# Kernel tuning notes

Hardware: AMD Instinct MI355X
Metric: run time of the kernel (lower is better)

## Reference

```python
import jax, jax.numpy as jnp
import numpy as np

B, U, V = 2, 32, 2048
IN_DIM, STATE, CODE = 256, 512, 256
H, HD = 8, 64
INNER = H * HD  # 512
HID = STATE     # ffn capacity_factor = 1.0


def layernorm(x, g, b, eps=1e-5):
    mu = jnp.mean(x, axis=-1, keepdims=True)
    var = jnp.var(x, axis=-1, keepdims=True)
    return (x - mu) * jax.lax.rsqrt(var + eps) * g + b


def setup_inputs() -> dict:
    key = jax.random.key(0)
    ks = jax.random.split(key, 24)
    s = 0.02
    inp = {
        'receiver_states': jax.random.normal(ks[0], (B, U, STATE), jnp.float32),
        'receiver_signatures': jax.random.normal(ks[1], (B, U, 64), jnp.float32),
        'receiver_codes': jax.random.normal(ks[2], (B, U, CODE), jnp.float32),
        'sender_states': jax.random.normal(ks[3], (B, V, IN_DIM), jnp.float32),
        # layernorms
        'ln_s_g': jnp.ones((IN_DIM,), jnp.float32), 'ln_s_b': jnp.zeros((IN_DIM,), jnp.float32),
        'ln_r_g': jnp.ones((STATE,), jnp.float32), 'ln_r_b': jnp.zeros((STATE,), jnp.float32),
        # ModFC query: in=STATE out=INNER ctx=CODE
        'Wq': jax.random.normal(ks[4], (INNER, STATE), jnp.float32) * s,
        'bq': jnp.zeros((INNER,), jnp.float32),
        'Cq': jax.random.normal(ks[5], (STATE, CODE), jnp.float32) * s,
        # ModFC key/value: in=IN_DIM out=INNER ctx=CODE
        'Wk': jax.random.normal(ks[6], (INNER, IN_DIM), jnp.float32) * s,
        'bk': jnp.zeros((INNER,), jnp.float32),
        'Ck': jax.random.normal(ks[7], (IN_DIM, CODE), jnp.float32) * s,
        'Wv': jax.random.normal(ks[8], (INNER, IN_DIM), jnp.float32) * s,
        'bv': jnp.zeros((INNER,), jnp.float32),
        'Cv': jax.random.normal(ks[9], (IN_DIM, CODE), jnp.float32) * s,
        # exit ModFC: in=INNER out=STATE ctx=CODE
        'We': jax.random.normal(ks[10], (STATE, INNER), jnp.float32) * s,
        'be': jnp.zeros((STATE,), jnp.float32),
        'Ce': jax.random.normal(ks[11], (INNER, CODE), jnp.float32) * s,
        'ls_attn': jnp.ones((STATE,), jnp.float32) * 1.0,
        # FFN
        'ln_f_g': jnp.ones((STATE,), jnp.float32), 'ln_f_b': jnp.zeros((STATE,), jnp.float32),
        'W1': jax.random.normal(ks[12], (HID, STATE), jnp.float32) * s,
        'b1': jnp.zeros((HID,), jnp.float32),
        'C1': jax.random.normal(ks[13], (STATE, CODE), jnp.float32) * s,
        'W2': jax.random.normal(ks[14], (STATE, HID), jnp.float32) * s,
        'b2': jnp.zeros((STATE,), jnp.float32),
        'C2': jax.random.normal(ks[15], (HID, CODE), jnp.float32) * s,
        'ls_ffn': jnp.ones((STATE,), jnp.float32) * 1e-6,
    }
    return inp


def reference(receiver_states, receiver_signatures, receiver_codes, sender_states,
              ln_s_g, ln_s_b, ln_r_g, ln_r_b,
              Wq, bq, Cq, Wk, bk, Ck, Wv, bv, Cv, We, be, Ce, ls_attn,
              ln_f_g, ln_f_b, W1, b1, C1, W2, b2, C2, ls_ffn):
    codes = receiver_codes  # (b,u,code)
    # --- ReadInAttention ---
    r_ln = layernorm(receiver_states, ln_r_g, ln_r_b)           # (b,u,state)
    s_ln = layernorm(sender_states, ln_s_g, ln_s_b)             # (b,v,in)
    # ModFC: y = linear(x * (1 + code @ C))
    # queries: (b,u,inner)
    q = jnp.einsum('bus,is->bui', r_ln * (1.0 + jnp.einsum('buc,sc->bus', codes, Cq)), Wq) + bq
    # per-receiver modulated senders: scale (b,u,in) broadcast over v
    scale_k = 1.0 + jnp.einsum('buc,ic->bui', codes, Ck)        # (b,u,in)
    scale_v = 1.0 + jnp.einsum('buc,ic->bui', codes, Cv)        # (b,u,in)
    mod_k = s_ln[:, :, None, :] * scale_k[:, None, :, :]        # (b,v,u,in)
    mod_v = s_ln[:, :, None, :] * scale_v[:, None, :, :]        # (b,v,u,in)
    keys = jnp.einsum('bvui,oi->bvuo', mod_k, Wk) + bk          # (b,v,u,inner)
    values = jnp.einsum('bvui,oi->bvuo', mod_v, Wv) + bv        # (b,v,u,inner)
    keys = keys.reshape(B, V, U, H, HD).transpose(0, 3, 2, 1, 4)    # (b,h,u,v,c)
    values = values.reshape(B, V, U, H, HD).transpose(0, 3, 2, 1, 4)
    qh = q.reshape(B, U, H, HD).transpose(0, 2, 1, 3)           # (b,h,u,c)
    scores = jnp.einsum('bhuc,bhuvc->bhuv', qh, keys) / np.sqrt(HD)
    attn = jax.nn.softmax(scores, axis=-1)
    msg = jnp.einsum('bhuv,bhuvc->bhuc', attn, values)          # (b,h,u,c)
    msg = msg.transpose(0, 2, 1, 3).reshape(B, U, INNER)        # (b,u,inner)
    msg = jnp.einsum('bui,oi->buo', msg * (1.0 + jnp.einsum('buc,ic->bui', codes, Ce)), We) + be
    attn_out = msg * ls_attn  # include_residual=False in read-in attention
    # --- ModFFN (residual) ---
    x = attn_out
    r = layernorm(x, ln_f_g, ln_f_b)
    h1 = jnp.einsum('bus,os->buo', r * (1.0 + jnp.einsum('buc,sc->bus', codes, C1)), W1) + b1
    h1 = jax.nn.gelu(h1, approximate=False)
    h2 = jnp.einsum('buh,oh->buo', h1 * (1.0 + jnp.einsum('buc,hc->buh', codes, C2)), W2) + b2
    out = x + h2 * ls_ffn
    return out
```

## Files before the change

kernel.cpp:

```cpp
#include <hip/hip_runtime.h>
#include <math.h>

#define B_ 2
#define U_ 32
#define V_ 2048
#define IN_ 256
#define ST_ 512
#define H_ 8
#define BU_ 64
#define NR_ 512

#define WS_SLN   0u
#define WS_SLNT  1048576u
#define WS_SCALE 2097152u
#define WS_T     2260992u
#define WS_CB    2392064u
#define WS_SSUMP 2392576u
#define WS_CTXP  2396672u
#define WS_AO    3445248u
#define WS_H2    3478016u
#define WS_AOP   3510784u

__device__ __forceinline__ float wsum(float v){
  #pragma unroll
  for(int m=32;m>0;m>>=1) v += __shfl_xor(v, m, 64);
  return v;
}

#define FMA4(A, t, S) { A.x += (t)*(S).x; A.y += (t)*(S).y; A.z += (t)*(S).z; A.w += (t)*(S).w; }

__global__ __launch_bounds__(256) void k_pre(const float* __restrict__ snd,
    const float* __restrict__ g, const float* __restrict__ bb,
    const float* __restrict__ codes,
    const float* __restrict__ Cq, const float* __restrict__ Ck, const float* __restrict__ Cv,
    const float* __restrict__ Ce, const float* __restrict__ C1, const float* __restrict__ C2,
    float* __restrict__ ws){
  __shared__ float tile[32][261];
  __shared__ float cds[8][256];
  const int tid = threadIdx.x;
  if(blockIdx.x < 128){
    const int wave = tid>>6, lane = tid&63;
    const int rowbase = blockIdx.x * 32;
    const int b = rowbase >> 11, vloc = rowbase & 2047;
    float4 gg  = *(const float4*)(g  + lane*4);
    float4 bbv = *(const float4*)(bb + lane*4);
    for(int it=0; it<8; ++it){
      int rl = it*4 + wave;
      int r  = rowbase + rl;
      float4 x = *(const float4*)(snd + (size_t)r*IN_ + lane*4);
      float s = x.x+x.y+x.z+x.w;
      float q = x.x*x.x+x.y*x.y+x.z*x.z+x.w*x.w;
      s = wsum(s); q = wsum(q);
      float mu = s*(1.0f/256.0f);
      float rv = rsqrtf(q*(1.0f/256.0f) - mu*mu + 1e-5f);
      float4 y;
      y.x = (x.x-mu)*rv*gg.x + bbv.x;
      y.y = (x.y-mu)*rv*gg.y + bbv.y;
      y.z = (x.z-mu)*rv*gg.z + bbv.z;
      y.w = (x.w-mu)*rv*gg.w + bbv.w;
      *(float4*)(ws + WS_SLN + (size_t)r*IN_ + lane*4) = y;
      tile[rl][lane*4+0] = y.x;
      tile[rl][lane*4+1] = y.y;
      tile[rl][lane*4+2] = y.z;
      tile[rl][lane*4+3] = y.w;
    }
    __syncthreads();
    const int vh = tid & 31;
    const int ibase = (tid >> 5);
    for(int it=0; it<32; ++it){
      int i = it*8 + ibase;
      ws[WS_SLNT + ((size_t)b*IN_ + i)*V_ + vloc + vh] = tile[vh][i];
    }
  } else {
    const int idx = blockIdx.x - 128;
    const int cg = idx % 40, bg = idx / 40;
    #pragma unroll
    for(int j=0;j<8;++j){
      int fi = j*256 + tid;
      cds[fi>>8][fi&255] = codes[(size_t)(bg*8)*256 + fi];
    }
    __syncthreads();
    const int q = tid & 3;
    const int col = cg*64 + (tid >> 2);
    const float* Cp; int loc;
    if(col < 512){ Cp = Cq; loc = col; }
    else if(col < 768){ Cp = Ck; loc = col - 512; }
    else if(col < 1024){ Cp = Cv; loc = col - 768; }
    else if(col < 1536){ Cp = Ce; loc = col - 1024; }
    else if(col < 2048){ Cp = C1; loc = col - 1536; }
    else { Cp = C2; loc = col - 2048; }
    const float4* wrow = (const float4*)(Cp + (size_t)loc*256 + q*64);
    float acc[8] = {0,0,0,0,0,0,0,0};
    #pragma unroll 4
    for(int i=0;i<16;++i){
      float4 w = wrow[i];
      #pragma unroll
      for(int k=0;k<8;++k){
        const float4 c = *(const float4*)(&cds[k][q*64 + i*4]);
        acc[k] += w.x*c.x + w.y*c.y + w.z*c.z + w.w*c.w;
      }
    }
    #pragma unroll
    for(int k=0;k<8;++k){
      acc[k] += __shfl_xor(acc[k], 1, 64);
      acc[k] += __shfl_xor(acc[k], 2, 64);
    }
    ws[WS_SCALE + (size_t)(bg*8 + q)*2560 + col]     = 1.0f + acc[q];
    ws[WS_SCALE + (size_t)(bg*8 + q + 4)*2560 + col] = 1.0f + acc[q+4];
  }
}

__global__ __launch_bounds__(256) void k_qt(const float* __restrict__ rst,
    const float* __restrict__ lg, const float* __restrict__ lb,
    const float* __restrict__ Wq, const float* __restrict__ bq,
    const float* __restrict__ Wk, const float* __restrict__ bk,
    float* __restrict__ ws){
  const int bu = blockIdx.x >> 3, h = blockIdx.x & 7;
  const int b = bu >> 5, u = bu & 31;
  const int r = (b*8 + h)*32 + u;
  const int tid = threadIdx.x, wave = tid>>6, lane = tid&63;
  __shared__ float xm[512];
  __shared__ float qv[64];
  __shared__ float red[4][65];
  __shared__ float rsm[4], rqm[4];
  float2 x2 = *(const float2*)(rst + (size_t)bu*512 + tid*2);
  float s = x2.x + x2.y, q = x2.x*x2.x + x2.y*x2.y;
  s = wsum(s); q = wsum(q);
  if(lane==0){ rsm[wave] = s; rqm[wave] = q; }
  __syncthreads();
  float S = rsm[0]+rsm[1]+rsm[2]+rsm[3];
  float Q = rqm[0]+rqm[1]+rqm[2]+rqm[3];
  float mu = S*(1.0f/512.0f);
  float rv = rsqrtf(Q*(1.0f/512.0f) - mu*mu + 1e-5f);
  const float* scal = ws + WS_SCALE + (size_t)bu*2560;
  xm[tid*2]   = ((x2.x-mu)*rv*lg[tid*2]   + lb[tid*2])   * scal[tid*2];
  xm[tid*2+1] = ((x2.y-mu)*rv*lg[tid*2+1] + lb[tid*2+1]) * scal[tid*2+1];
  __syncthreads();
  {
    const int o = tid & 63, sp = tid >> 6;
    const float4* wq = (const float4*)(Wq + (size_t)(h*64 + o)*512 + sp*128);
    const float* xp = xm + sp*128;
    float acc = 0.f;
    #pragma unroll 8
    for(int c4=0;c4<32;++c4){
      float4 w = wq[c4];
      acc += w.x*xp[c4*4] + w.y*xp[c4*4+1] + w.z*xp[c4*4+2] + w.w*xp[c4*4+3];
    }
    red[sp][o] = acc;
  }
  __syncthreads();
  if(tid < 64)
    qv[tid] = red[0][tid]+red[1][tid]+red[2][tid]+red[3][tid] + bq[h*64+tid];
  __syncthreads();
  if(tid < 64){
    float p = qv[tid] * bk[h*64+tid];
    p = wsum(p);
    if(tid==0) ws[WS_CB + r] = p;
  }
  {
    float acc = 0.f;
    #pragma unroll 4
    for(int d=0; d<64; ++d)
      acc += qv[d] * Wk[(size_t)(h*64+d)*256 + tid];
    ws[WS_T + (size_t)r*256 + tid] = acc * scal[512 + tid];
  }
}

__global__ __launch_bounds__(512) void k_scctx(const float* __restrict__ Tm, float* __restrict__ ws){
  const int rg = blockIdx.x >> 3, vc = blockIdx.x & 7;
  const int r0 = rg * 8;
  const int b  = rg >> 5;
  const int v0 = vc * 256;
  const int tid = threadIdx.x, lane = tid & 63;
  const int w  = __builtin_amdgcn_readfirstlane(tid >> 6);
  const int wr = w & 1, wk = w >> 1;
  const int rw4 = wr * 4;
  const int i0 = lane * 4;
  const int srow = tid >> 6;
  const int sf   = (tid & 63) * 4;

  __shared__ float P[8][256];
  __shared__ float stg[32][256];

  float4 a0={0,0,0,0},a1={0,0,0,0},a2={0,0,0,0},a3={0,0,0,0};
  const float* Trow = Tm + (size_t)(r0 + rw4)*256;

  const float* p1base = ws + WS_SLNT + (size_t)b*IN_*V_ + v0;
  float4 g0,g1,g2,g3;
  g0 = *(const float4*)(p1base + (size_t)(srow    )*V_ + sf);
  g1 = *(const float4*)(p1base + (size_t)(srow+ 8)*V_ + sf);
  g2 = *(const float4*)(p1base + (size_t)(srow+16)*V_ + sf);
  g3 = *(const float4*)(p1base + (size_t)(srow+24)*V_ + sf);
  for(int s=0; s<8; ++s){
    __syncthreads();
    *(float4*)&stg[srow   ][sf] = g0;
    *(float4*)&stg[srow+ 8][sf] = g1;
    *(float4*)&stg[srow+16][sf] = g2;
    *(float4*)&stg[srow+24][sf] = g3;
    if(s < 7){
      const float* nb = p1base + (size_t)(s+1)*32*V_;
      g0 = *(const float4*)(nb + (size_t)(srow    )*V_ + sf);
      g1 = *(const float4*)(nb + (size_t)(srow+ 8)*V_ + sf);
      g2 = *(const float4*)(nb + (size_t)(srow+16)*V_ + sf);
      g3 = *(const float4*)(nb + (size_t)(srow+24)*V_ + sf);
    }
    const int kgA = s*32 + wk*8;
    float4 tA[4], tB[4];
    #pragma unroll
    for(int j=0;j<4;++j) tA[j] = *(const float4*)(Trow + (size_t)j*256 + kgA);
    __syncthreads();
    #pragma unroll
    for(int j=0;j<4;++j) tB[j] = *(const float4*)(Trow + (size_t)j*256 + kgA + 4);
    {
      const int kl = wk*8;
      float4 s0 = *(const float4*)&stg[kl+0][i0];
// ... 86 lines not shown
      FMA4(a3,p3_.x,s0) FMA4(a3,p3_.y,s1) FMA4(a3,p3_.z,s2) FMA4(a3,p3_.w,s3)
    }
  }
  __syncthreads();
  if(wk == 0){
    *(float4*)&P[rw4+0][i0]=a0; *(float4*)&P[rw4+1][i0]=a1;
    *(float4*)&P[rw4+2][i0]=a2; *(float4*)&P[rw4+3][i0]=a3;
  } else if(wk == 1){
    *(float4*)&stg[rw4+0][i0]=a0; *(float4*)&stg[rw4+1][i0]=a1;
    *(float4*)&stg[rw4+2][i0]=a2; *(float4*)&stg[rw4+3][i0]=a3;
  } else if(wk == 2){
    *(float4*)&stg[8+rw4+0][i0]=a0; *(float4*)&stg[8+rw4+1][i0]=a1;
    *(float4*)&stg[8+rw4+2][i0]=a2; *(float4*)&stg[8+rw4+3][i0]=a3;
  }
  __syncthreads();
  if(wk == 3){
    float4 av[4] = {a0,a1,a2,a3};
    #pragma unroll
    for(int j=0;j<4;++j){
      const int r = r0 + rw4 + j;
      float4 q0 = *(const float4*)&P[rw4+j][i0];
      float4 q1 = *(const float4*)&stg[rw4+j][i0];
      float4 q2 = *(const float4*)&stg[8+rw4+j][i0];
      float4 d;
      d.x = av[j].x+q0.x+q1.x+q2.x;
      d.y = av[j].y+q0.y+q1.y+q2.y;
      d.z = av[j].z+q0.z+q1.z+q2.z;
      d.w = av[j].w+q0.w+q1.w+q2.w;
      *(float4*)(ws + WS_CTXP + ((size_t)vc*NR_ + r)*IN_ + i0) = d;
    }
  }
}

__global__ __launch_bounds__(512) void k_mexit(const float* __restrict__ Wv, const float* __restrict__ bv,
    const float* __restrict__ We, float* __restrict__ ws){
  const int bu = blockIdx.x >> 2, st = blockIdx.x & 3;
  const int b = bu >> 5, u = bu & 31;
  const int tid = threadIdx.x;
  __shared__ float xs[2][256];
  __shared__ float m2s[128];
  __shared__ float ps[4][128];
  __shared__ float invS[2];
  if(tid < 2){
    const int r = (b*8 + st*2 + tid)*32 + u;
    float v = 0.f;
    #pragma unroll
    for(int k=0;k<8;++k) v += ws[WS_SSUMP + (size_t)r*8 + k];
    invS[tid] = 1.0f / v;
  }
  {
    const int hh = tid >> 8, i = tid & 255;
    const int r = (b*8 + st*2 + hh)*32 + u;
    float s = 0.f;
    #pragma unroll
    for(int vcx=0; vcx<8; ++vcx)
      s += ws[WS_CTXP + ((size_t)vcx*NR_ + r)*IN_ + i];
    xs[hh][i] = s * ws[WS_SCALE + (size_t)bu*2560 + 768 + i];
  }
  __syncthreads();
  {
    const int lo = tid & 127, sp = tid >> 7;
    const int o = st*128 + lo;
    const float4* wv = (const float4*)(Wv + (size_t)o*256 + sp*64);
    const float* xp = &xs[lo>>6][sp*64];
    float acc = 0.f;
    #pragma unroll
    for(int c4=0;c4<16;++c4){
      float4 w = wv[c4];
      acc += w.x*xp[c4*4]+w.y*xp[c4*4+1]+w.z*xp[c4*4+2]+w.w*xp[c4*4+3];
    }
    ps[sp][lo] = acc;
  }
  __syncthreads();
  if(tid < 128){
    const int o = st*128 + tid;
    m2s[tid] = ((ps[0][tid]+ps[1][tid]+ps[2][tid]+ps[3][tid]) * invS[tid>>6] + bv[o])
               * ws[WS_SCALE + (size_t)bu*2560 + 1024 + o];
  }
  __syncthreads();
  {
    const float4* we = (const float4*)(We + (size_t)tid*512 + st*128);
    float acc = 0.f;
    #pragma unroll 8
    for(int c4=0;c4<32;++c4){
      float4 w = we[c4];
      acc += w.x*m2s[c4*4]+w.y*m2s[c4*4+1]+w.z*m2s[c4*4+2]+w.w*m2s[c4*4+3];
    }
    ws[WS_AOP + ((size_t)st*BU_ + bu)*512 + tid] = acc;
  }
}

__global__ __launch_bounds__(256) void k_ffn1(const float* __restrict__ be, const float* __restrict__ lsa,
    const float* __restrict__ lg, const float* __restrict__ lb,
    const float* __restrict__ W1, const float* __restrict__ b1, float* __restrict__ ws){
  const int bu = blockIdx.x >> 2, ot = blockIdx.x & 3;
  const int tid = threadIdx.x, wave = tid>>6, lane = tid&63;
  __shared__ float xr[512];
  __shared__ float rsm[4], rqm[4];
  __shared__ float ps[2][128];
  const int s2 = tid*2;
  float2 x2;
  {
    const float* aop = ws + WS_AOP;
    float ax = aop[((size_t)0*BU_+bu)*512+s2] + aop[((size_t)1*BU_+bu)*512+s2]
             + aop[((size_t)2*BU_+bu)*512+s2] + aop[((size_t)3*BU_+bu)*512+s2];
    float ay = aop[((size_t)0*BU_+bu)*512+s2+1] + aop[((size_t)1*BU_+bu)*512+s2+1]
             + aop[((size_t)2*BU_+bu)*512+s2+1] + aop[((size_t)3*BU_+bu)*512+s2+1];
    x2.x = (ax + be[s2])   * lsa[s2];
    x2.y = (ay + be[s2+1]) * lsa[s2+1];
    *(float2*)(ws + WS_AO + (size_t)bu*512 + s2) = x2;
  }
  float s = x2.x+x2.y, q = x2.x*x2.x+x2.y*x2.y;
  s = wsum(s); q = wsum(q);
  if(lane==0){ rsm[wave]=s; rqm[wave]=q; }
  __syncthreads();
  float S=rsm[0]+rsm[1]+rsm[2]+rsm[3], Q=rqm[0]+rqm[1]+rqm[2]+rqm[3];
  float mu = S*(1.0f/512.0f);
  float rv = rsqrtf(Q*(1.0f/512.0f) - mu*mu + 1e-5f);
  const float* scal = ws + WS_SCALE + (size_t)bu*2560;
  xr[s2]   = ((x2.x-mu)*rv*lg[s2]   + lb[s2])   * scal[1536 + s2];
  xr[s2+1] = ((x2.y-mu)*rv*lg[s2+1] + lb[s2+1]) * scal[1536 + s2+1];
  __syncthreads();
  const int o = ot*128 + (tid & 127), sp = tid >> 7;
  const float4* w1 = (const float4*)(W1 + (size_t)o*512 + sp*256);
  const float* xp = xr + sp*256;
  float acc = 0.f;
  #pragma unroll 8
  for(int c4=0;c4<64;++c4){
    float4 w = w1[c4];
    acc += w.x*xp[c4*4]+w.y*xp[c4*4+1]+w.z*xp[c4*4+2]+w.w*xp[c4*4+3];
  }
  ps[sp][tid&127] = acc;
  __syncthreads();
  if(sp==0){
    float hh = ps[0][tid] + ps[1][tid] + b1[o];
    float ge = 0.5f*hh*(1.0f + erff(hh*0.70710678118654752f));
    ws[WS_H2 + (size_t)bu*512 + o] = ge * scal[2048 + o];
  }
}

__global__ __launch_bounds__(256) void k_ffn2(const float* __restrict__ W2, const float* __restrict__ b2,
    const float* __restrict__ lsf, const float* __restrict__ ws, float* __restrict__ out){
  const int bu = blockIdx.x >> 2, st = blockIdx.x & 3;
  const int tid = threadIdx.x;
  const int s = st*128 + (tid & 127), sp = tid >> 7;
  __shared__ float ps[2][128];
  const float4* w2 = (const float4*)(W2 + (size_t)s*512 + sp*256);
  const float* hp = ws + WS_H2 + (size_t)bu*512 + sp*256;
  float acc = 0.f;
  #pragma unroll 8
  for(int c4=0;c4<64;++c4){
    float4 w = w2[c4];
    acc += w.x*hp[c4*4]+w.y*hp[c4*4+1]+w.z*hp[c4*4+2]+w.w*hp[c4*4+3];
  }
  ps[sp][tid&127] = acc;
  __syncthreads();
  if(sp==0)
    out[(size_t)bu*512 + s] = ws[WS_AO + (size_t)bu*512 + s]
                            + (ps[0][tid]+ps[1][tid] + b2[s]) * lsf[s];
}

extern "C" void kernel_launch(void* const* d_in, const int* in_sizes, int n_in,
                              void* d_out, int out_size, void* d_ws, size_t ws_size,
                              hipStream_t stream) {
  (void)in_sizes; (void)n_in; (void)out_size; (void)ws_size;
  const float* rst   = (const float*)d_in[0];
  const float* codes = (const float*)d_in[2];
  const float* snd   = (const float*)d_in[3];
  const float* ln_s_g = (const float*)d_in[4];
  const float* ln_s_b = (const float*)d_in[5];
  const float* ln_r_g = (const float*)d_in[6];
  const float* ln_r_b = (const float*)d_in[7];
  const float* Wq = (const float*)d_in[8];
  const float* bq = (const float*)d_in[9];
  const float* Cq = (const float*)d_in[10];
  const float* Wk = (const float*)d_in[11];
  const float* bk = (const float*)d_in[12];
  const float* Ck = (const float*)d_in[13];
  const float* Wv = (const float*)d_in[14];
  const float* bv = (const float*)d_in[15];
  const float* Cv = (const float*)d_in[16];
  const float* We = (const float*)d_in[17];
  const float* be = (const float*)d_in[18];
  const float* Ce = (const float*)d_in[19];
  const float* lsa = (const float*)d_in[20];
  const float* ln_f_g = (const float*)d_in[21];
  const float* ln_f_b = (const float*)d_in[22];
  const float* W1 = (const float*)d_in[23];
  const float* b1 = (const float*)d_in[24];
  const float* C1 = (const float*)d_in[25];
  const float* W2 = (const float*)d_in[26];
  const float* b2 = (const float*)d_in[27];
  const float* C2 = (const float*)d_in[28];
  const float* lsf = (const float*)d_in[29];
  float* ws  = (float*)d_ws;
  float* out = (float*)d_out;

  k_pre   <<<448, 256, 0, stream>>>(snd, ln_s_g, ln_s_b, codes, Cq, Ck, Cv, Ce, C1, C2, ws);
  k_qt    <<<512, 256, 0, stream>>>(rst, ln_r_g, ln_r_b, Wq, bq, Wk, bk, ws);
  k_scctx <<<512, 512, 0, stream>>>((const float*)(ws + WS_T), ws);
  k_mexit <<<256, 512, 0, stream>>>(Wv, bv, We, ws);
  k_ffn1  <<<256, 256, 0, stream>>>(be, lsa, ln_f_g, ln_f_b, W1, b1, ws);
  k_ffn2  <<<256, 256, 0, stream>>>(W2, b2, lsf, ws, out);
}
```

Before: 94.18 us.

## Fuse query/T prep into preprocessing kernel and collapse tail into one per-row kernel

Merges the code-scale computation, receiver layernorm, query projection and key-fold (T) into the sender-layernorm kernel, and fuses value projection, exit projection and both FFN layers into a single per-(b,u) kernel. This cuts the launch count from six to three and removes global round trips through the workspace for scales, attention-out partials and FFN hidden state. The cost is far fewer blocks in the tail (64) and in the query path (64 blocks of 512 threads), each doing full 512x512 matvecs serially. That lowers parallelism and spreads weight reads across only 64 CUs.

After: 240.2 us. +155.0%, slower.

```diff
diff --git a/kernel.cpp b/kernel.cpp
--- a/kernel.cpp
+++ b/kernel.cpp
@@ -12,14 +12,10 @@
 
 #define WS_SLN   0u
 #define WS_SLNT  1048576u
-#define WS_SCALE 2097152u
 #define WS_T     2260992u
 #define WS_CB    2392064u
 #define WS_SSUMP 2392576u
 #define WS_CTXP  2396672u
-#define WS_AO    3445248u
-#define WS_H2    3478016u
-#define WS_AOP   3510784u
 
 __device__ __forceinline__ float wsum(float v){
   #pragma unroll
@@ -29,23 +25,30 @@
 
 #define FMA4(A, t, S) { A.x += (t)*(S).x; A.y += (t)*(S).y; A.z += (t)*(S).z; A.w += (t)*(S).w; }
 
-__global__ __launch_bounds__(256) void k_pre(const float* __restrict__ snd,
-    const float* __restrict__ g, const float* __restrict__ bb,
+__global__ __launch_bounds__(512) void k_pre2(
+    const float* __restrict__ snd, const float* __restrict__ sg, const float* __restrict__ sb,
+    const float* __restrict__ rst, const float* __restrict__ rg, const float* __restrict__ rb,
     const float* __restrict__ codes,
-    const float* __restrict__ Cq, const float* __restrict__ Ck, const float* __restrict__ Cv,
-    const float* __restrict__ Ce, const float* __restrict__ C1, const float* __restrict__ C2,
+    const float* __restrict__ Cq, const float* __restrict__ Ck,
+    const float* __restrict__ Wq, const float* __restrict__ bq,
+    const float* __restrict__ Wk, const float* __restrict__ bk,
     float* __restrict__ ws){
   __shared__ float tile[32][261];
-  __shared__ float cds[8][256];
-  const int tid = threadIdx.x;
+  __shared__ float cds[256];
+  __shared__ float scq[512];
+  __shared__ float sck[256];
+  __shared__ float xm[512];
+  __shared__ float qv[512];
+  __shared__ float rsm[8], rqm[8];
+  const int tid = threadIdx.x, lane = tid & 63, wave = tid >> 6;
   if(blockIdx.x < 128){
-    const int wave = tid>>6, lane = tid&63;
     const int rowbase = blockIdx.x * 32;
     const int b = rowbase >> 11, vloc = rowbase & 2047;
-    float4 gg  = *(const float4*)(g  + lane*4);
-    float4 bbv = *(const float4*)(bb + lane*4);
-    for(int it=0; it<8; ++it){
-      int rl = it*4 + wave;
+    float4 gg  = *(const float4*)(sg + lane*4);
+    float4 bbv = *(const float4*)(sb + lane*4);
+    #pragma unroll
+    for(int it=0; it<4; ++it){
+      int rl = it*8 + wave;
       int r  = rowbase + rl;
       float4 x = *(const float4*)(snd + (size_t)r*IN_ + lane*4);
       float s = x.x+x.y+x.z+x.w;
@@ -65,104 +68,85 @@
       tile[rl][lane*4+3] = y.w;
     }
     __syncthreads();
-    const int vh = tid & 31;
-    const int ibase = (tid >> 5);
-    for(int it=0; it<32; ++it){
-      int i = it*8 + ibase;
+    const int vh = tid & 31, ig = tid >> 5;
+    #pragma unroll
+    for(int it=0; it<16; ++it){
+      int i = it*16 + ig;
       ws[WS_SLNT + ((size_t)b*IN_ + i)*V_ + vloc + vh] = tile[vh][i];
     }
   } else {
-    const int idx = blockIdx.x - 128;
-    const int cg = idx % 40, bg = idx / 40;
-    #pragma unroll
-    for(int j=0;j<8;++j){
-      int fi = j*256 + tid;
-      cds[fi>>8][fi&255] = codes[(size_t)(bg*8)*256 + fi];
-    }
-    __syncthreads();
-    const int q = tid & 3;
-    const int col = cg*64 + (tid >> 2);
-    const float* Cp; int loc;
-    if(col < 512){ Cp = Cq; loc = col; }
-    else if(col < 768){ Cp = Ck; loc = col - 512; }
-    else if(col < 1024){ Cp = Cv; loc = col - 768; }
-    else if(col < 1536){ Cp = Ce; loc = col - 1024; }
-    else if(col < 2048){ Cp = C1; loc = col - 1536; }
-    else { Cp = C2; loc = col - 2048; }
-    const float4* wrow = (const float4*)(Cp + (size_t)loc*256 + q*64);
-    float acc[8] = {0,0,0,0,0,0,0,0};
-    #pragma unroll 4
-    for(int i=0;i<16;++i){
-      float4 w = wrow[i];
+    const int bu = blockIdx.x - 128;
+    const int b = bu >> 5, u = bu & 31;
+    if(tid < 64) *(float4*)&cds[tid*4] = *(const float4*)(codes + (size_t)bu*256 + tid*4);
+    __syncthreads();
+    {
+      const int q4 = tid & 3, ci = tid >> 2;
       #pragma unroll
-      for(int k=0;k<8;++k){
-        const float4 c = *(const float4*)(&cds[k][q*64 + i*4]);
-        acc[k] += w.x*c.x + w.y*c.y + w.z*c.z + w.w*c.w;
+      for(int p=0; p<6; ++p){
+        const int col = p*128 + ci;
+        const float* Crow = (col < 512) ? (Cq + (size_t)col*256) : (Ck + (size_t)(col-512)*256);
+        const float4* cr = (const float4*)Crow + q4*16;
+        float acc = 0.f;
+        #pragma unroll
+        for(int i=0;i<16;++i){
+          float4 w = cr[i];
+          const float4 c = *(const float4*)&cds[q4*64 + i*4];
+          acc += w.x*c.x + w.y*c.y + w.z*c.z + w.w*c.w;
+        }
+        acc += __shfl_xor(acc,1,64); acc += __shfl_xor(acc,2,64);
+        if(q4==0){ if(col<512) scq[col] = 1.f+acc; else sck[col-512] = 1.f+acc; }
       }
     }
-    #pragma unroll
-    for(int k=0;k<8;++k){
-      acc[k] += __shfl_xor(acc[k], 1, 64);
-      acc[k] += __shfl_xor(acc[k], 2, 64);
-    }
-    ws[WS_SCALE + (size_t)(bg*8 + q)*2560 + col]     = 1.0f + acc[q];
-    ws[WS_SCALE + (size_t)(bg*8 + q + 4)*2560 + col] = 1.0f + acc[q+4];
-  }
-}
-
-__global__ __launch_bounds__(256) void k_qt(const float* __restrict__ rst,
-    const float* __restrict__ lg, const float* __restrict__ lb,
-    const float* __restrict__ Wq, const float* __restrict__ bq,
-    const float* __restrict__ Wk, const float* __restrict__ bk,
-    float* __restrict__ ws){
-  const int bu = blockIdx.x >> 3, h = blockIdx.x & 7;
-  const int b = bu >> 5, u = bu & 31;
-  const int r = (b*8 + h)*32 + u;
-  const int tid = threadIdx.x, wave = tid>>6, lane = tid&63;
-  __shared__ float xm[512];
-  __shared__ float qv[64];
-  __shared__ float red[4][65];
-  __shared__ float rsm[4], rqm[4];
-  float2 x2 = *(const float2*)(rst + (size_t)bu*512 + tid*2);
-  float s = x2.x + x2.y, q = x2.x*x2.x + x2.y*x2.y;
-  s = wsum(s); q = wsum(q);
-  if(lane==0){ rsm[wave] = s; rqm[wave] = q; }
-  __syncthreads();
-  float S = rsm[0]+rsm[1]+rsm[2]+rsm[3];
-  float Q = rqm[0]+rqm[1]+rqm[2]+rqm[3];
-  float mu = S*(1.0f/512.0f);
-  float rv = rsqrtf(Q*(1.0f/512.0f) - mu*mu + 1e-5f);
-  const float* scal = ws + WS_SCALE + (size_t)bu*2560;
-  xm[tid*2]   = ((x2.x-mu)*rv*lg[tid*2]   + lb[tid*2])   * scal[tid*2];
-  xm[tid*2+1] = ((x2.y-mu)*rv*lg[tid*2+1] + lb[tid*2+1]) * scal[tid*2+1];
-  __syncthreads();
-  {
-    const int o = tid & 63, sp = tid >> 6;
-    const float4* wq = (const float4*)(Wq + (size_t)(h*64 + o)*512 + sp*128);
-    const float* xp = xm + sp*128;
-    float acc = 0.f;
-    #pragma unroll 8
-    for(int c4=0;c4<32;++c4){
-      float4 w = wq[c4];
-      acc += w.x*xp[c4*4] + w.y*xp[c4*4+1] + w.z*xp[c4*4+2] + w.w*xp[c4*4+3];
-    }
-    red[sp][o] = acc;
-  }
-  __syncthreads();
-  if(tid < 64)
-    qv[tid] = red[0][tid]+red[1][tid]+red[2][tid]+red[3][tid] + bq[h*64+tid];
-  __syncthreads();
-  if(tid < 64){
-    float p = qv[tid] * bk[h*64+tid];
-    p = wsum(p);
-    if(tid==0) ws[WS_CB + r] = p;
-  }
-  {
-    float acc = 0.f;
-    #pragma unroll 4
-    for(int d=0; d<64; ++d)
-      acc += qv[d] * Wk[(size_t)(h*64+d)*256 + tid];
-    ws[WS_T + (size_t)r*256 + tid] = acc * scal[512 + tid];
+    float xv = rst[(size_t)bu*512 + tid];
+    {
+      float s = wsum(xv), q2 = wsum(xv*xv);
+      if(lane==0){ rsm[wave]=s; rqm[wave]=q2; }
+    }
+    __syncthreads();
+    {
+      float S=0.f, Q=0.f;
+      #pragma unroll
+      for(int k=0;k<8;++k){ S+=rsm[k]; Q+=rqm[k]; }
+      float mu = S*(1.0f/512.0f);
+      float rv = rsqrtf(Q*(1.0f/512.0f) - mu*mu + 1e-5f);
+      xm[tid] = ((xv-mu)*rv*rg[tid] + rb[tid]) * scq[tid];
+    }
+    __syncthreads();
+    {
+      const float4* wq = (const float4*)(Wq + (size_t)tid*512);
+      float acc = 0.f;
+      #pragma unroll 8
+      for(int c4=0;c4<128;++c4){
+        float4 w = wq[c4];
+        acc += w.x*xm[c4*4]+w.y*xm[c4*4+1]+w.z*xm[c4*4+2]+w.w*xm[c4*4+3];
+      }
+      qv[tid] = acc + bq[tid];
+    }
+    __syncthreads();
+    if(tid < 64){
+      const int h = lane >> 3, ks = lane & 7;
+      float p = 0.f;
+      #pragma unroll
+      for(int j=0;j<8;++j){
+        const int d = h*64 + ks*8 + j;
+        p += qv[d] * bk[d];
+      }
+      p += __shfl_xor(p,1,64); p += __shfl_xor(p,2,64); p += __shfl_xor(p,4,64);
+      if(ks==0) ws[WS_CB + (size_t)((b*8+h)*32+u)] = p;
+    }
+    {
+      const int h = tid >> 6, i0 = (tid & 63)*4;
+      float4 acc = {0,0,0,0};
+      #pragma unroll 4
+      for(int d=0; d<64; ++d){
+        const float qd = qv[h*64 + d];
+        float4 w = *(const float4*)(Wk + (size_t)(h*64+d)*256 + i0);
+        acc.x += qd*w.x; acc.y += qd*w.y; acc.z += qd*w.z; acc.w += qd*w.w;
+      }
+      float4 sc = *(const float4*)&sck[i0];
+      acc.x*=sc.x; acc.y*=sc.y; acc.z*=sc.z; acc.w*=sc.w;
+      *(float4*)(ws + WS_T + (size_t)((b*8+h)*32+u)*256 + i0) = acc;
+    }
   }
 }
 
@@ -333,132 +317,138 @@
   }
 }
 
-__global__ __launch_bounds__(512) void k_mexit(const float* __restrict__ Wv, const float* __restrict__ bv,
-    const float* __restrict__ We, float* __restrict__ ws){
-  const int bu = blockIdx.x >> 2, st = blockIdx.x & 3;
-  const int b = bu >> 5, u = bu & 31;
-  const int tid = threadIdx.x;
-  __shared__ float xs[2][256];
-  __shared__ float m2s[128];
-  __shared__ float ps[4][128];
-  __shared__ float invS[2];
-  if(tid < 2){
-    const int r = (b*8 + st*2 + tid)*32 + u;
-    float v = 0.f;
-    #pragma unroll
-    for(int k=0;k<8;++k) v += ws[WS_SSUMP + (size_t)r*8 + k];
-    invS[tid] = 1.0f / v;
-  }
-  {
-    const int hh = tid >> 8, i = tid & 255;
-    const int r = (b*8 + st*2 + hh)*32 + u;
-    float s = 0.f;
-    #pragma unroll
-    for(int vcx=0; vcx<8; ++vcx)
-      s += ws[WS_CTXP + ((size_t)vcx*NR_ + r)*IN_ + i];
-    xs[hh][i] = s * ws[WS_SCALE + (size_t)bu*2560 + 768 + i];
-  }
-  __syncthreads();
-  {
-    const int lo = tid & 127, sp = tid >> 7;
-    const int o = st*128 + lo;
-    const float4* wv = (const float4*)(Wv + (size_t)o*256 + sp*64);
-    const float* xp = &xs[lo>>6][sp*64];
+__global__ __launch_bounds__(512) void k_tail(
+    const float* __restrict__ codes,
+    const float* __restrict__ Cv, const float* __restrict__ Ce,
+    const float* __restrict__ C1, const float* __restrict__ C2,
+    const float* __restrict__ Wv, const float* __restrict__ bv,
+    const float* __restrict__ We, const float* __restrict__ be,
+    const float* __restrict__ lsa,
+    const float* __restrict__ fg, const float* __restrict__ fb,
+    const float* __restrict__ W1, const float* __restrict__ b1,
+    const float* __restrict__ W2, const float* __restrict__ b2,
+    const float* __restrict__ lsf,
+    float* __restrict__ ws, float* __restrict__ out){
+  __shared__ float cds[256];
+  __shared__ float scv[256];
+  __shared__ float sce[512];
+  __shared__ float scf1[512];
+  __shared__ float scf2[512];
+  __shared__ float xs[8][256];
+  __shared__ float m2[512];
+  __shared__ float aoL[512];
+  __shared__ float xr[512];
+  __shared__ float h2[512];
+  __shared__ float invS[8];
+  __shared__ float rsm[8], rqm[8];
+  const int tid = threadIdx.x, lane = tid & 63, wave = tid >> 6;
+  const int bu = blockIdx.x, b = bu >> 5, u = bu & 31;
+  if(tid < 64) *(float4*)&cds[tid*4] = *(const float4*)(codes + (size_t)bu*256 + tid*4);
+  __syncthreads();
+  {
+    const int q4 = tid & 3, ci = tid >> 2;
+    #pragma unroll
+    for(int p=0; p<14; ++p){
+      const int col = p*128 + ci;
+      const float* Crow; float* dst; int loc;
+      if(col < 256){ Crow = Cv + (size_t)col*256; dst = scv; loc = col; }
+      else if(col < 768){ Crow = Ce + (size_t)(col-256)*256; dst = sce; loc = col-256; }
+      else if(col < 1280){ Crow = C1 + (size_t)(col-768)*256; dst = scf1; loc = col-768; }
+      else { Crow = C2 + (size_t)(col-1280)*256; dst = scf2; loc = col-1280; }
+      const float4* cr = (const float4*)Crow + q4*16;
+      float acc = 0.f;
+      #pragma unroll
+      for(int i=0;i<16;++i){
+        float4 w = cr[i];
+        const float4 c = *(const float4*)&cds[q4*64 + i*4];
+        acc += w.x*c.x + w.y*c.y + w.z*c.z + w.w*c.w;
+      }
+      acc += __shfl_xor(acc,1,64); acc += __shfl_xor(acc,2,64);
+      if(q4==0) dst[loc] = 1.f + acc;
+    }
+  }
+  if(tid < 64){
+    const int h = lane >> 3, k = lane & 7;
+    const int r = (b*8+h)*32 + u;
+    float v = ws[WS_SSUMP + (size_t)r*8 + k];
+    v += __shfl_xor(v,1,64); v += __shfl_xor(v,2,64); v += __shfl_xor(v,4,64);
+    if(k==0) invS[h] = 1.f/v;
+  }
+  __syncthreads();
+  {
+    const int h = tid >> 6, i0 = (tid & 63)*4;
+    const int r = (b*8+h)*32 + u;
+    float4 sacc = {0,0,0,0};
+    #pragma unroll
+    for(int vcx=0; vcx<8; ++vcx){
+      float4 t = *(const float4*)(ws + WS_CTXP + ((size_t)vcx*NR_ + r)*IN_ + i0);
+      sacc.x+=t.x; sacc.y+=t.y; sacc.z+=t.z; sacc.w+=t.w;
+    }
+    float4 sc = *(const float4*)&scv[i0];
+    sacc.x*=sc.x; sacc.y*=sc.y; sacc.z*=sc.z; sacc.w*=sc.w;
+    *(float4*)&xs[h][i0] = sacc;
+  }
+  __syncthreads();
+  {
+    const int h = tid >> 6;
+    const float4* wv = (const float4*)(Wv + (size_t)tid*256);
+    const float* xp = &xs[h][0];
     float acc = 0.f;
-    #pragma unroll
-    for(int c4=0;c4<16;++c4){
+    #pragma unroll 8
+    for(int c4=0;c4<64;++c4){
       float4 w = wv[c4];
       acc += w.x*xp[c4*4]+w.y*xp[c4*4+1]+w.z*xp[c4*4+2]+w.w*xp[c4*4+3];
     }
-    ps[sp][lo] = acc;
-  }
-  __syncthreads();
-  if(tid < 128){
-    const int o = st*128 + tid;
-    m2s[tid] = ((ps[0][tid]+ps[1][tid]+ps[2][tid]+ps[3][tid]) * invS[tid>>6] + bv[o])
-               * ws[WS_SCALE + (size_t)bu*2560 + 1024 + o];
-  }
-  __syncthreads();
-  {
-    const float4* we = (const float4*)(We + (size_t)tid*512 + st*128);
+    m2[tid] = (acc*invS[h] + bv[tid]) * sce[tid];
+  }
+  __syncthreads();
+  {
+    const float4* we = (const float4*)(We + (size_t)tid*512);
     float acc = 0.f;
     #pragma unroll 8
-    for(int c4=0;c4<32;++c4){
+    for(int c4=0;c4<128;++c4){
       float4 w = we[c4];
-      acc += w.x*m2s[c4*4]+w.y*m2s[c4*4+1]+w.z*m2s[c4*4+2]+w.w*m2s[c4*4+3];
-    }
-    ws[WS_AOP + ((size_t)st*BU_ + bu)*512 + tid] = acc;
-  }
-}
-
-__global__ __launch_bounds__(256) void k_ffn1(const float* __restrict__ be, const float* __restrict__ lsa,
-    const float* __restrict__ lg, const float* __restrict__ lb,
-    const float* __restrict__ W1, const float* __restrict__ b1, float* __restrict__ ws){
-  const int bu = blockIdx.x >> 2, ot = blockIdx.x & 3;
-  const int tid = threadIdx.x, wave = tid>>6, lane = tid&63;
-  __shared__ float xr[512];
-  __shared__ float rsm[4], rqm[4];
-  __shared__ float ps[2][128];
-  const int s2 = tid*2;
-  float2 x2;
-  {
-    const float* aop = ws + WS_AOP;
-    float ax = aop[((size_t)0*BU_+bu)*512+s2] + aop[((size_t)1*BU_+bu)*512+s2]
-             + aop[((size_t)2*BU_+bu)*512+s2] + aop[((size_t)3*BU_+bu)*512+s2];
-    float ay = aop[((size_t)0*BU_+bu)*512+s2+1] + aop[((size_t)1*BU_+bu)*512+s2+1]
-             + aop[((size_t)2*BU_+bu)*512+s2+1] + aop[((size_t)3*BU_+bu)*512+s2+1];
-    x2.x = (ax + be[s2])   * lsa[s2];
-    x2.y = (ay + be[s2+1]) * lsa[s2+1];
-    *(float2*)(ws + WS_AO + (size_t)bu*512 + s2) = x2;
-  }
-  float s = x2.x+x2.y, q = x2.x*x2.x+x2.y*x2.y;
-  s = wsum(s); q = wsum(q);
-  if(lane==0){ rsm[wave]=s; rqm[wave]=q; }
-  __syncthreads();
-  float S=rsm[0]+rsm[1]+rsm[2]+rsm[3], Q=rqm[0]+rqm[1]+rqm[2]+rqm[3];
-  float mu = S*(1.0f/512.0f);
-  float rv = rsqrtf(Q*(1.0f/512.0f) - mu*mu + 1e-5f);
-  const float* scal = ws + WS_SCALE + (size_t)bu*2560;
-  xr[s2]   = ((x2.x-mu)*rv*lg[s2]   + lb[s2])   * scal[1536 + s2];
-  xr[s2+1] = ((x2.y-mu)*rv*lg[s2+1] + lb[s2+1]) * scal[1536 + s2+1];
-  __syncthreads();
-  const int o = ot*128 + (tid & 127), sp = tid >> 7;
-  const float4* w1 = (const float4*)(W1 + (size_t)o*512 + sp*256);
-  const float* xp = xr + sp*256;
-  float acc = 0.f;
-  #pragma unroll 8
-  for(int c4=0;c4<64;++c4){
-    float4 w = w1[c4];
-    acc += w.x*xp[c4*4]+w.y*xp[c4*4+1]+w.z*xp[c4*4+2]+w.w*xp[c4*4+3];
-  }
-  ps[sp][tid&127] = acc;
-  __syncthreads();
-  if(sp==0){
-    float hh = ps[0][tid] + ps[1][tid] + b1[o];
+      acc += w.x*m2[c4*4]+w.y*m2[c4*4+1]+w.z*m2[c4*4+2]+w.w*m2[c4*4+3];
+    }
+    aoL[tid] = (acc + be[tid]) * lsa[tid];
+  }
+  __syncthreads();
+  {
+    float xv = aoL[tid];
+    float s = wsum(xv), q2 = wsum(xv*xv);
+    if(lane==0){ rsm[wave]=s; rqm[wave]=q2; }
+    __syncthreads();
+    float S=0.f, Q=0.f;
+    #pragma unroll
+    for(int k=0;k<8;++k){ S+=rsm[k]; Q+=rqm[k]; }
+    float mu = S*(1.0f/512.0f);
+    float rv = rsqrtf(Q*(1.0f/512.0f) - mu*mu + 1e-5f);
+    xr[tid] = ((xv-mu)*rv*fg[tid] + fb[tid]) * scf1[tid];
+  }
+  __syncthreads();
+  {
+    const float4* w1 = (const float4*)(W1 + (size_t)tid*512);
+    float acc = 0.f;
+    #pragma unroll 8
+    for(int c4=0;c4<128;++c4){
+      float4 w = w1[c4];
+      acc += w.x*xr[c4*4]+w.y*xr[c4*4+1]+w.z*xr[c4*4+2]+w.w*xr[c4*4+3];
+    }
+    float hh = acc + b1[tid];
     float ge = 0.5f*hh*(1.0f + erff(hh*0.70710678118654752f));
-    ws[WS_H2 + (size_t)bu*512 + o] = ge * scal[2048 + o];
-  }
-}
-
-__global__ __launch_bounds__(256) void k_ffn2(const float* __restrict__ W2, const float* __restrict__ b2,
-    const float* __restrict__ lsf, const float* __restrict__ ws, float* __restrict__ out){
-  const int bu = blockIdx.x >> 2, st = blockIdx.x & 3;
-  const int tid = threadIdx.x;
-  const int s = st*128 + (tid & 127), sp = tid >> 7;
-  __shared__ float ps[2][128];
-  const float4* w2 = (const float4*)(W2 + (size_t)s*512 + sp*256);
-  const float* hp = ws + WS_H2 + (size_t)bu*512 + sp*256;
-  float acc = 0.f;
-  #pragma unroll 8
-  for(int c4=0;c4<64;++c4){
-    float4 w = w2[c4];
-    acc += w.x*hp[c4*4]+w.y*hp[c4*4+1]+w.z*hp[c4*4+2]+w.w*hp[c4*4+3];
-  }
-  ps[sp][tid&127] = acc;
-  __syncthreads();
-  if(sp==0)
-    out[(size_t)bu*512 + s] = ws[WS_AO + (size_t)bu*512 + s]
-                            + (ps[0][tid]+ps[1][tid] + b2[s]) * lsf[s];
+    h2[tid] = ge * scf2[tid];
+  }
+  __syncthreads();
+  {
+    const float4* w2 = (const float4*)(W2 + (size_t)tid*512);
+    float acc = 0.f;
+    #pragma unroll 8
+    for(int c4=0;c4<128;++c4){
+      float4 w = w2[c4];
+      acc += w.x*h2[c4*4]+w.y*h2[c4*4+1]+w.z*h2[c4*4+2]+w.w*h2[c4*4+3];
+    }
+    out[(size_t)bu*512 + tid] = aoL[tid] + (acc + b2[tid]) * lsf[tid];
+  }
 }
 
 extern "C" void kernel_launch(void* const* d_in, const int* in_sizes, int n_in,
@@ -497,10 +487,9 @@
   float* ws  = (float*)d_ws;
   float* out = (float*)d_out;
 
-  k_pre   <<<448, 256, 0, stream>>>(snd, ln_s_g, ln_s_b, codes, Cq, Ck, Cv, Ce, C1, C2, ws);
-  k_qt    <<<512, 256, 0, stream>>>(rst, ln_r_g, ln_r_b, Wq, bq, Wk, bk, ws);
+  k_pre2  <<<192, 512, 0, stream>>>(snd, ln_s_g, ln_s_b, rst, ln_r_g, ln_r_b,
+                                    codes, Cq, Ck, Wq, bq, Wk, bk, ws);
   k_scctx <<<512, 512, 0, stream>>>((const float*)(ws + WS_T), ws);
-  k_mexit <<<256, 512, 0, stream>>>(Wv, bv, We, ws);
-  k_ffn1  <<<256, 256, 0, stream>>>(be, lsa, ln_f_g, ln_f_b, W1, b1, ws);
-  k_ffn2  <<<256, 256, 0, stream>>>(W2, b2, lsf, ws, out);
+  k_tail  <<<64, 512, 0, stream>>>(codes, Cv, Ce, C1, C2, Wv, bv, We, be, lsa,
+                                   ln_f_g, ln_f_b, W1, b1, W2, b2, lsf, ws, out);
 }
```

## Fuse exit projection and FFN into one tail kernel, move code scales into scctx

Applied to the files above, without the earlier changes.

Replaces the three tail kernels (mexit, ffn1, ffn2) with a single k_tail4 kernel. Each of its 4 blocks per (b,u) row redundantly computes the full Wv, We, layernorm, W1 and GELU chain, then splits only the W2 output across blocks. The code-scale GEMV for Cv/Ce/C1/C2 moves from k_pre into extra blocks of k_scctx, since those scales are only needed later. This removes two launches and the workspace round trips, but each block now does four times the matvec work and weight reads for the earlier stages.

Result: slower. 143.1 us (+51.9%).

```diff
diff --git a/kernel.cpp b/kernel.cpp
--- a/kernel.cpp
+++ b/kernel.cpp
@@ -17,9 +17,6 @@
 #define WS_CB    2392064u
 #define WS_SSUMP 2392576u
 #define WS_CTXP  2396672u
-#define WS_AO    3445248u
-#define WS_H2    3478016u
-#define WS_AOP   3510784u
 
 __device__ __forceinline__ float wsum(float v){
   #pragma unroll
@@ -32,8 +29,7 @@
 __global__ __launch_bounds__(256) void k_pre(const float* __restrict__ snd,
     const float* __restrict__ g, const float* __restrict__ bb,
     const float* __restrict__ codes,
-    const float* __restrict__ Cq, const float* __restrict__ Ck, const float* __restrict__ Cv,
-    const float* __restrict__ Ce, const float* __restrict__ C1, const float* __restrict__ C2,
+    const float* __restrict__ Cq, const float* __restrict__ Ck,
     float* __restrict__ ws){
   __shared__ float tile[32][261];
   __shared__ float cds[8][256];
@@ -73,7 +69,7 @@
     }
   } else {
     const int idx = blockIdx.x - 128;
-    const int cg = idx % 40, bg = idx / 40;
+    const int cg = idx % 12, bg = idx / 12;
     #pragma unroll
     for(int j=0;j<8;++j){
       int fi = j*256 + tid;
@@ -84,11 +80,7 @@
     const int col = cg*64 + (tid >> 2);
     const float* Cp; int loc;
     if(col < 512){ Cp = Cq; loc = col; }
-    else if(col < 768){ Cp = Ck; loc = col - 512; }
-    else if(col < 1024){ Cp = Cv; loc = col - 768; }
-    else if(col < 1536){ Cp = Ce; loc = col - 1024; }
-    else if(col < 2048){ Cp = C1; loc = col - 1536; }
-    else { Cp = C2; loc = col - 2048; }
+    else { Cp = Ck; loc = col - 512; }
     const float4* wrow = (const float4*)(Cp + (size_t)loc*256 + q*64);
     float acc[8] = {0,0,0,0,0,0,0,0};
     #pragma unroll 4
@@ -166,21 +158,61 @@
   }
 }
 
-__global__ __launch_bounds__(512) void k_scctx(const float* __restrict__ Tm, float* __restrict__ ws){
+__global__ __launch_bounds__(512) void k_scctx(const float* __restrict__ Tm,
+    const float* __restrict__ codes,
+    const float* __restrict__ Cv, const float* __restrict__ Ce,
+    const float* __restrict__ C1, const float* __restrict__ C2,
+    float* __restrict__ ws){
+  __shared__ float P[8][256];
+  __shared__ float stg[32][256];
+  __shared__ float cds8[8][256];
+  const int tid = threadIdx.x, lane = tid & 63;
+  if(blockIdx.x >= 512){
+    const int idx = blockIdx.x - 512;
+    const int bg = idx / 14, cc = idx % 14;
+    #pragma unroll
+    for(int j=0;j<4;++j){
+      int fi = j*512 + tid;
+      cds8[fi>>8][fi&255] = codes[(size_t)(bg*8)*256 + fi];
+    }
+    __syncthreads();
+    const int q4 = tid & 3;
+    const int col = 768 + cc*128 + (tid >> 2);
+    const float* Cp; int loc;
+    if(col < 1024){ Cp = Cv; loc = col - 768; }
+    else if(col < 1536){ Cp = Ce; loc = col - 1024; }
+    else if(col < 2048){ Cp = C1; loc = col - 1536; }
+    else { Cp = C2; loc = col - 2048; }
+    const float4* wrow = (const float4*)(Cp + (size_t)loc*256 + q4*64);
+    float acc[8] = {0,0,0,0,0,0,0,0};
+    #pragma unroll 4
+    for(int i=0;i<16;++i){
+      float4 w = wrow[i];
+      #pragma unroll
+      for(int k=0;k<8;++k){
+        const float4 c = *(const float4*)(&cds8[k][q4*64 + i*4]);
+        acc[k] += w.x*c.x + w.y*c.y + w.z*c.z + w.w*c.w;
+      }
+    }
+    #pragma unroll
+    for(int k=0;k<8;++k){
+      acc[k] += __shfl_xor(acc[k], 1, 64);
+      acc[k] += __shfl_xor(acc[k], 2, 64);
+    }
+    ws[WS_SCALE + (size_t)(bg*8 + q4)*2560 + col]     = 1.0f + acc[q4];
+    ws[WS_SCALE + (size_t)(bg*8 + q4 + 4)*2560 + col] = 1.0f + acc[q4+4];
+    return;
+  }
   const int rg = blockIdx.x >> 3, vc = blockIdx.x & 7;
   const int r0 = rg * 8;
   const int b  = rg >> 5;
   const int v0 = vc * 256;
-  const int tid = threadIdx.x, lane = tid & 63;
   const int w  = __builtin_amdgcn_readfirstlane(tid >> 6);
   const int wr = w & 1, wk = w >> 1;
   const int rw4 = wr * 4;
   const int i0 = lane * 4;
   const int srow = tid >> 6;
   const int sf   = (tid & 63) * 4;
-
-  __shared__ float P[8][256];
-  __shared__ float stg[32][256];
 
   float4 a0={0,0,0,0},a1={0,0,0,0},a2={0,0,0,0},a3={0,0,0,0};
   const float* Trow = Tm + (size_t)(r0 + rw4)*256;
@@ -333,132 +365,117 @@
   }
 }
 
-__global__ __launch_bounds__(512) void k_mexit(const float* __restrict__ Wv, const float* __restrict__ bv,
-    const float* __restrict__ We, float* __restrict__ ws){
+__global__ __launch_bounds__(512) void k_tail4(
+    const float* __restrict__ Wv, const float* __restrict__ bv,
+    const float* __restrict__ We, const float* __restrict__ be,
+    const float* __restrict__ lsa,
+    const float* __restrict__ fg, const float* __restrict__ fb,
+    const float* __restrict__ W1, const float* __restrict__ b1,
+    const float* __restrict__ W2, const float* __restrict__ b2,
+    const float* __restrict__ lsf,
+    float* __restrict__ ws, float* __restrict__ out){
+  __shared__ float xs[8][256];
+  __shared__ float m2[512];
+  __shared__ float aoL[512];
+  __shared__ float xr[512];
+  __shared__ float h2[512];
+  __shared__ float invS[8];
+  __shared__ float rsm[8], rqm[8];
+  __shared__ float ps[4][128];
+  const int tid = threadIdx.x, lane = tid & 63, wave = tid >> 6;
   const int bu = blockIdx.x >> 2, st = blockIdx.x & 3;
   const int b = bu >> 5, u = bu & 31;
-  const int tid = threadIdx.x;
-  __shared__ float xs[2][256];
-  __shared__ float m2s[128];
-  __shared__ float ps[4][128];
-  __shared__ float invS[2];
-  if(tid < 2){
-    const int r = (b*8 + st*2 + tid)*32 + u;
-    float v = 0.f;
-    #pragma unroll
-    for(int k=0;k<8;++k) v += ws[WS_SSUMP + (size_t)r*8 + k];
-    invS[tid] = 1.0f / v;
-  }
-  {
-    const int hh = tid >> 8, i = tid & 255;
-    const int r = (b*8 + st*2 + hh)*32 + u;
-    float s = 0.f;
-    #pragma unroll
-    for(int vcx=0; vcx<8; ++vcx)
-      s += ws[WS_CTXP + ((size_t)vcx*NR_ + r)*IN_ + i];
-    xs[hh][i] = s * ws[WS_SCALE + (size_t)bu*2560 + 768 + i];
+  const float* scal = ws + WS_SCALE + (size_t)bu*2560;
+  if(tid < 64){
+    const int h = lane >> 3, k = lane & 7;
+    const int r = (b*8+h)*32 + u;
+    float v = ws[WS_SSUMP + (size_t)r*8 + k];
+    v += __shfl_xor(v,1,64); v += __shfl_xor(v,2,64); v += __shfl_xor(v,4,64);
+    if(k==0) invS[h] = 1.f/v;
+  }
+  {
+    const int h = tid >> 6, i0 = (tid & 63)*4;
+    const int r = (b*8+h)*32 + u;
+    float4 sacc = {0,0,0,0};
+    #pragma unroll
+    for(int vcx=0; vcx<8; ++vcx){
+      float4 t = *(const float4*)(ws + WS_CTXP + ((size_t)vcx*NR_ + r)*IN_ + i0);
+      sacc.x+=t.x; sacc.y+=t.y; sacc.z+=t.z; sacc.w+=t.w;
+    }
+    float4 sc = *(const float4*)(scal + 768 + i0);
+    sacc.x*=sc.x; sacc.y*=sc.y; sacc.z*=sc.z; sacc.w*=sc.w;
+    *(float4*)&xs[h][i0] = sacc;
+  }
+  __syncthreads();
+  {
+    const int h = tid >> 6;
+    const float4* wv = (const float4*)(Wv + (size_t)tid*256);
+    const float* xp = &xs[h][0];
+    float acc = 0.f;
+    #pragma unroll 8
+    for(int c4=0;c4<64;++c4){
+      float4 w = wv[c4];
+      acc += w.x*xp[c4*4]+w.y*xp[c4*4+1]+w.z*xp[c4*4+2]+w.w*xp[c4*4+3];
+    }
+    m2[tid] = (acc*invS[h] + bv[tid]) * scal[1024 + tid];
+  }
+  __syncthreads();
+  {
+    const float4* we = (const float4*)(We + (size_t)tid*512);
+    float acc = 0.f;
+    #pragma unroll 8
+    for(int c4=0;c4<128;++c4){
+      float4 w = we[c4];
+      acc += w.x*m2[c4*4]+w.y*m2[c4*4+1]+w.z*m2[c4*4+2]+w.w*m2[c4*4+3];
+    }
+    aoL[tid] = (acc + be[tid]) * lsa[tid];
+  }
+  __syncthreads();
+  {
+    float xv = aoL[tid];
+    float s = wsum(xv), q2 = wsum(xv*xv);
+    if(lane==0){ rsm[wave]=s; rqm[wave]=q2; }
+    __syncthreads();
+    float S=0.f, Q=0.f;
+    #pragma unroll
+    for(int k=0;k<8;++k){ S+=rsm[k]; Q+=rqm[k]; }
+    float mu = S*(1.0f/512.0f);
+    float rv = rsqrtf(Q*(1.0f/512.0f) - mu*mu + 1e-5f);
+    xr[tid] = ((xv-mu)*rv*fg[tid] + fb[tid]) * scal[1536 + tid];
+  }
+  __syncthreads();
+  {
+    const float4* w1 = (const float4*)(W1 + (size_t)tid*512);
+    float acc = 0.f;
+    #pragma unroll 8
+    for(int c4=0;c4<128;++c4){
+      float4 w = w1[c4];
+      acc += w.x*xr[c4*4]+w.y*xr[c4*4+1]+w.z*xr[c4*4+2]+w.w*xr[c4*4+3];
+    }
+    float hh = acc + b1[tid];
+    float ge = 0.5f*hh*(1.0f + erff(hh*0.70710678118654752f));
+    h2[tid] = ge * scal[2048 + tid];
   }
   __syncthreads();
   {
     const int lo = tid & 127, sp = tid >> 7;
     const int o = st*128 + lo;
-    const float4* wv = (const float4*)(Wv + (size_t)o*256 + sp*64);
-    const float* xp = &xs[lo>>6][sp*64];
-    float acc = 0.f;
-    #pragma unroll
-    for(int c4=0;c4<16;++c4){
-      float4 w = wv[c4];
-      acc += w.x*xp[c4*4]+w.y*xp[c4*4+1]+w.z*xp[c4*4+2]+w.w*xp[c4*4+3];
-    }
-    ps[sp][lo] = acc;
-  }
-  __syncthreads();
-  if(tid < 128){
-    const int o = st*128 + tid;
-    m2s[tid] = ((ps[0][tid]+ps[1][tid]+ps[2][tid]+ps[3][tid]) * invS[tid>>6] + bv[o])
-               * ws[WS_SCALE + (size_t)bu*2560 + 1024 + o];
-  }
-  __syncthreads();
-  {
-    const float4* we = (const float4*)(We + (size_t)tid*512 + st*128);
+    const float4* w2 = (const float4*)(W2 + (size_t)o*512 + sp*128);
+    const float* hp = h2 + sp*128;
     float acc = 0.f;
     #pragma unroll 8
     for(int c4=0;c4<32;++c4){
-      float4 w = we[c4];
-      acc += w.x*m2s[c4*4]+w.y*m2s[c4*4+1]+w.z*m2s[c4*4+2]+w.w*m2s[c4*4+3];
-    }
-    ws[WS_AOP + ((size_t)st*BU_ + bu)*512 + tid] = acc;
-  }
-}
-
-__global__ __launch_bounds__(256) void k_ffn1(const float* __restrict__ be, const float* __restrict__ lsa,
-    const float* __restrict__ lg, const float* __restrict__ lb,
-    const float* __restrict__ W1, const float* __restrict__ b1, float* __restrict__ ws){
-  const int bu = blockIdx.x >> 2, ot = blockIdx.x & 3;
-  const int tid = threadIdx.x, wave = tid>>6, lane = tid&63;
-  __shared__ float xr[512];
-  __shared__ float rsm[4], rqm[4];
-  __shared__ float ps[2][128];
-  const int s2 = tid*2;
-  float2 x2;
-  {
-    const float* aop = ws + WS_AOP;
-    float ax = aop[((size_t)0*BU_+bu)*512+s2] + aop[((size_t)1*BU_+bu)*512+s2]
-             + aop[((size_t)2*BU_+bu)*512+s2] + aop[((size_t)3*BU_+bu)*512+s2];
-    float ay = aop[((size_t)0*BU_+bu)*512+s2+1] + aop[((size_t)1*BU_+bu)*512+s2+1]
-             + aop[((size_t)2*BU_+bu)*512+s2+1] + aop[((size_t)3*BU_+bu)*512+s2+1];
-    x2.x = (ax + be[s2])   * lsa[s2];
-    x2.y = (ay + be[s2+1]) * lsa[s2+1];
-    *(float2*)(ws + WS_AO + (size_t)bu*512 + s2) = x2;
-  }
-  float s = x2.x+x2.y, q = x2.x*x2.x+x2.y*x2.y;
-  s = wsum(s); q = wsum(q);
-  if(lane==0){ rsm[wave]=s; rqm[wave]=q; }
-  __syncthreads();
-  float S=rsm[0]+rsm[1]+rsm[2]+rsm[3], Q=rqm[0]+rqm[1]+rqm[2]+rqm[3];
-  float mu = S*(1.0f/512.0f);
-  float rv = rsqrtf(Q*(1.0f/512.0f) - mu*mu + 1e-5f);
-  const float* scal = ws + WS_SCALE + (size_t)bu*2560;
-  xr[s2]   = ((x2.x-mu)*rv*lg[s2]   + lb[s2])   * scal[1536 + s2];
-  xr[s2+1] = ((x2.y-mu)*rv*lg[s2+1] + lb[s2+1]) * scal[1536 + s2+1];
-  __syncthreads();
-  const int o = ot*128 + (tid & 127), sp = tid >> 7;
-  const float4* w1 = (const float4*)(W1 + (size_t)o*512 + sp*256);
-  const float* xp = xr + sp*256;
-  float acc = 0.f;
-  #pragma unroll 8
-  for(int c4=0;c4<64;++c4){
-    float4 w = w1[c4];
-    acc += w.x*xp[c4*4]+w.y*xp[c4*4+1]+w.z*xp[c4*4+2]+w.w*xp[c4*4+3];
-  }
-  ps[sp][tid&127] = acc;
-  __syncthreads();
-  if(sp==0){
-    float hh = ps[0][tid] + ps[1][tid] + b1[o];
-    float ge = 0.5f*hh*(1.0f + erff(hh*0.70710678118654752f));
-    ws[WS_H2 + (size_t)bu*512 + o] = ge * scal[2048 + o];
-  }
-}
-
-__global__ __launch_bounds__(256) void k_ffn2(const float* __restrict__ W2, const float* __restrict__ b2,
-    const float* __restrict__ lsf, const float* __restrict__ ws, float* __restrict__ out){
-  const int bu = blockIdx.x >> 2, st = blockIdx.x & 3;
-  const int tid = threadIdx.x;
-  const int s = st*128 + (tid & 127), sp = tid >> 7;
-  __shared__ float ps[2][128];
-  const float4* w2 = (const float4*)(W2 + (size_t)s*512 + sp*256);
-  const float* hp = ws + WS_H2 + (size_t)bu*512 + sp*256;
-  float acc = 0.f;
-  #pragma unroll 8
-  for(int c4=0;c4<64;++c4){
-    float4 w = w2[c4];
-    acc += w.x*hp[c4*4]+w.y*hp[c4*4+1]+w.z*hp[c4*4+2]+w.w*hp[c4*4+3];
-  }
-  ps[sp][tid&127] = acc;
-  __syncthreads();
-  if(sp==0)
-    out[(size_t)bu*512 + s] = ws[WS_AO + (size_t)bu*512 + s]
-                            + (ps[0][tid]+ps[1][tid] + b2[s]) * lsf[s];
+      float4 w = w2[c4];
+      acc += w.x*hp[c4*4]+w.y*hp[c4*4+1]+w.z*hp[c4*4+2]+w.w*hp[c4*4+3];
+    }
+    ps[sp][lo] = acc;
+  }
+  __syncthreads();
+  if(tid < 128){
+    const int o = st*128 + tid;
+    out[(size_t)bu*512 + o] = aoL[o]
+      + (ps[0][tid]+ps[1][tid]+ps[2][tid]+ps[3][tid] + b2[o]) * lsf[o];
+  }
 }
 
 extern "C" void kernel_launch(void* const* d_in, const int* in_sizes, int n_in,
@@ -497,10 +514,9 @@
   float* ws  = (float*)d_ws;
   float* out = (float*)d_out;
 
-  k_pre   <<<448, 256, 0, stream>>>(snd, ln_s_g, ln_s_b, codes, Cq, Ck, Cv, Ce, C1, C2, ws);
+  k_pre   <<<224, 256, 0, stream>>>(snd, ln_s_g, ln_s_b, codes, Cq, Ck, ws);
   k_qt    <<<512, 256, 0, stream>>>(rst, ln_r_g, ln_r_b, Wq, bq, Wk, bk, ws);
-  k_scctx <<<512, 512, 0, stream>>>((const float*)(ws + WS_T), ws);
-  k_mexit <<<256, 512, 0, stream>>>(Wv, bv, We, ws);
-  k_ffn1  <<<256, 256, 0, stream>>>(be, lsa, ln_f_g, ln_f_b, W1, b1, ws);
-  k_ffn2  <<<256, 256, 0, stream>>>(W2, b2, lsf, ws, out);
+  k_scctx <<<624, 512, 0, stream>>>((const float*)(ws + WS_T), codes, Cv, Ce, C1, C2, ws);
+  k_tail4 <<<256, 512, 0, stream>>>(Wv, bv, We, be, lsa, ln_f_g, ln_f_b,
+                                    W1, b1, W2, b2, lsf, ws, out);
 }
```
